# Kernel optimization log

Measured on AMD Instinct MI355X. Metric: run time of the kernel, lower is better.

Reference implementation:

```python
import jax, jax.numpy as jnp
import numpy as np

C_CURV = 0.001
L = 10
N = 16
OMEGA = 1.0
EPS = 1e-6


def _fnmap(x, a0, a, b):
    # x: [M, C]; radial Fourier gate
    r = jnp.maximum(jnp.linalg.norm(x, axis=1, keepdims=True), EPS)  # [M,1]
    n = jnp.arange(1, N + 1, dtype=x.dtype)[None, :]                 # [1,N]
    angle = OMEGA * (r * n)                                          # [M,N]
    f_r = a0 + jnp.cos(angle) @ a[:, None] + jnp.sin(angle) @ b[:, None]  # [M,1]
    return f_r * x


def _log_map_origin(x, c):
    sc = jnp.sqrt(c)
    rn = jnp.maximum(jnp.linalg.norm(x, axis=1, keepdims=True), EPS)
    arg = jnp.minimum(sc * rn, 1.0 - 1e-5)
    return (jnp.arctanh(arg) / (sc * rn)) * x


def _exp_map_origin(v, c):
    sc = jnp.sqrt(c)
    rn = jnp.maximum(jnp.linalg.norm(v, axis=1, keepdims=True), EPS)
    return (jnp.tanh(sc * rn) / (sc * rn)) * v


def setup_inputs() -> dict:
    key = jax.random.key(0)
    ks = jax.random.split(key, 8)
    B, C, H, W = 32, 256, 64, 64
    x = jax.random.normal(ks[0], (B, C, H, W), dtype=jnp.float32) * 0.1
    inp = {
        "x": x,
        "a0_1": jnp.ones((1,), jnp.float32),
        "a_1": jax.random.normal(ks[1], (N,), jnp.float32) * 0.02,
        "b_1": jax.random.normal(ks[2], (N,), jnp.float32) * 0.02,
        "a0_2": jnp.ones((1,), jnp.float32),
        "a_2": jax.random.normal(ks[3], (N,), jnp.float32) * 0.02,
        "b_2": jax.random.normal(ks[4], (N,), jnp.float32) * 0.02,
        "phi": jax.random.normal(ks[5], (C,), jnp.float32) * 0.02,
        "alpha": jnp.ones((1,), jnp.float32),
        "beta": jnp.zeros((1,), jnp.float32),
    }
    return inp


def reference(x, a0_1, a_1, b_1, a0_2, a_2, b_2, phi, alpha, beta):
    B, C, H, W = x.shape
    h0 = jnp.transpose(x, (0, 2, 3, 1)).reshape(-1, C)  # [B*H*W, C]
    u = _log_map_origin(h0, C_CURV)
    u1 = _fnmap(u, a0_1, a_1, b_1)
    U = jnp.fft.rfft(u1, axis=1)                         # [M, C//2+1]
    ang = L * phi
    Hf = jax.lax.complex(jnp.cos(ang), jnp.sin(ang))     # [C]
    V = U * Hf[None, : U.shape[-1]]
    v0 = jnp.fft.irfft(V, n=C, axis=1)
    v1 = _fnmap(v0, a0_2, a_2, b_2)
    y = _exp_map_origin(v1, C_CURV)
    out = alpha * y + beta * h0
    return jnp.transpose(out.reshape(B, H, W, C), (0, 3, 1, 2))
```

## Files before the change

kernel.cpp:

```cpp
#include <hip/hip_runtime.h>
#include <math.h>

typedef __attribute__((ext_vector_type(8))) unsigned short ushort8;
typedef __attribute__((ext_vector_type(8))) __bf16 bf16x8;
typedef __attribute__((ext_vector_type(4))) float f32x4;

constexpr int   CDIM  = 256;
constexpr int   HWSP  = 4096;
constexpr int   PPB   = 64;
constexpr float SQRTC = 0.031622776601683794f;
constexpr float EPSR  = 1e-6f;

__device__ inline unsigned short f2bf(float x) {
    unsigned int u = __float_as_uint(x);
    u += 0x7FFFu + ((u >> 16) & 1u);
    return (unsigned short)(u >> 16);
}

__global__ void build_wpk(const float* __restrict__ phi,
                          unsigned short* __restrict__ wpk) {
    __shared__ float w[256];
    const int d = threadIdx.x;
    {
        const float step = 6.283185307179586f / 256.0f;
        double s = 0.0;
        for (int k = 1; k <= 127; ++k) {
            int kd = (k * d) & 255;
            s += 2.0 * (double)cosf(10.0f * phi[k] + step * (float)kd);
        }
        s += (double)cosf(10.0f * phi[0]);
        double c128 = (double)cosf(10.0f * phi[128]);
        s += (d & 1) ? -c128 : c128;
        w[d] = (float)(s * (1.0 / 256.0));
    }
    __syncthreads();
    const int l = d & 63, q = d >> 6;
    for (int blk = q; blk < 128; blk += 4) {
        const int outc = (blk & 15) * 16 + (l & 15);
        const int ch0  = (blk >> 4) * 32 + (l >> 4) * 8;
        ushort8 u;
        #pragma unroll
        for (int j = 0; j < 8; ++j)
            u[j] = f2bf(w[(outc - (ch0 + j)) & 255]);
        *reinterpret_cast<ushort8*>(&wpk[(size_t)(blk * 64 + l) * 8]) = u;
    }
}

__device__ inline float fourier_gate(float r, float A0,
                                     const float* __restrict__ a,
                                     const float* __restrict__ b) {
    float sn, cs;
    sincosf(r, &sn, &cs);
    float c = cs, s = sn, f = A0;
    #pragma unroll
    for (int n = 0; n < 16; ++n) {
        f = fmaf(a[n], c, f);
        f = fmaf(b[n], s, f);
        float c2 = fmaf(c, cs, -s * sn);
        float s2 = fmaf(s, cs,  c * sn);
        c = c2; s = s2;
    }
    return f;
}

__global__ __launch_bounds__(256, 4)
void fused_mfma(const float* __restrict__ x,
                const float* __restrict__ a0_1, const float* __restrict__ a1,
                const float* __restrict__ b1,
                const float* __restrict__ a0_2, const float* __restrict__ a2,
                const float* __restrict__ b2,
                const float* __restrict__ phi,
                const float* __restrict__ alpha, const float* __restrict__ beta,
                const unsigned short* __restrict__ wpk,
                float* __restrict__ out) {
    __shared__ __align__(16) unsigned short Xl[PPB][CDIM];
    __shared__ __align__(16) float stats[3][4][PPB];
    __shared__ __align__(16) float sobuf[PPB];

    const int t  = threadIdx.x;
    const int l  = t & 63;
    const int g  = t >> 6;
    const int lr = l & 15;
    const int lk = l >> 4;
    const int b  = blockIdx.x >> 6;
    const int s0 = (blockIdx.x & 63) * PPB;
    const float* xb = x + (size_t)b * CDIM * HWSP + s0;

    f32x4 vns = {0.f,0.f,0.f,0.f}, vs0 = {0.f,0.f,0.f,0.f}, vsa = {0.f,0.f,0.f,0.f};
    const int posq = t & 15;
    #pragma unroll
    for (int i = 0; i < 2; ++i) {
        const int co = i * 16 + (t >> 4);
        f32x4 v[8];
        #pragma unroll
        for (int j = 0; j < 8; ++j)
            v[j] = *reinterpret_cast<const f32x4*>(
                       &xb[(size_t)(co * 8 + j) * HWSP + posq * 4]);
        #pragma unroll
        for (int j = 0; j < 8; ++j) {
            vns += v[j] * v[j];
            vs0 += v[j];
            vsa  = (j & 1) ? vsa - v[j] : vsa + v[j];
        }
        #pragma unroll
        for (int r = 0; r < 4; ++r) {
            ushort8 u;
            #pragma unroll
            for (int j = 0; j < 8; ++j) u[j] = f2bf(v[j][r]);
            const int pos = posq * 4 + r;
            *reinterpret_cast<ushort8*>(&Xl[pos][(co * 8) ^ ((pos & 15) << 3)]) = u;
        }
    }
    #pragma unroll
    for (int r = 0; r < 4; ++r) {
        float aa = vns[r], ss = vs0[r], mm = vsa[r];
        aa += __shfl_xor(aa, 16, 64); aa += __shfl_xor(aa, 32, 64);
        ss += __shfl_xor(ss, 16, 64); ss += __shfl_xor(ss, 32, 64);
        mm += __shfl_xor(mm, 16, 64); mm += __shfl_xor(mm, 32, 64);
        vns[r] = aa; vs0[r] = ss; vsa[r] = mm;
    }
    if (lk == 0) {
        *reinterpret_cast<f32x4*>(&stats[0][g][posq * 4]) = vns;
        *reinterpret_cast<f32x4*>(&stats[1][g][posq * 4]) = vs0;
        *reinterpret_cast<f32x4*>(&stats[2][g][posq * 4]) = vsa;
    }
    __syncthreads();

    if (t < PPB) {
        float nsq = stats[0][0][t] + stats[0][1][t] + stats[0][2][t] + stats[0][3][t];
        float S0  = stats[1][0][t] + stats[1][1][t] + stats[1][2][t] + stats[1][3][t];
        float Sa  = stats[2][0][t] + stats[2][1][t] + stats[2][2][t] + stats[2][3][t];
        float sin0 = sinf(10.0f * phi[0]);
        float sinN = sinf(10.0f * phi[128]);
        float n0  = sqrtf(nsq);
        float rn0 = fmaxf(n0, EPSR);
        float arg = fminf(SQRTC * rn0, 1.0f - 1e-5f);
        float ls  = atanhf(arg) / (SQRTC * rn0);
        float r1  = fmaxf(ls * n0, EPSR);
        float s1  = ls * fourier_gate(r1, a0_1[0], a1, b1);
        float dn2 = fmaxf(nsq - (S0 * S0 * sin0 * sin0 + Sa * Sa * sinN * sinN)
                                 * (1.0f / 256.0f), 0.f);
        float nv  = sqrtf(dn2) * fabsf(s1);
        float r2  = fmaxf(nv, EPSR);
        float f2  = fourier_gate(r2, a0_2[0], a2, b2);
        float rn1 = fmaxf(fabsf(f2) * nv, EPSR);
        float es  = tanhf(SQRTC * rn1) / (SQRTC * rn1);
        sobuf[t]  = alpha[0] * es * f2 * s1;
    }

    f32x4 acc[4][4];
    #pragma unroll
    for (int m = 0; m < 4; ++m)
        #pragma unroll
        for (int n = 0; n < 4; ++n)
            acc[m][n] = f32x4{0.f, 0.f, 0.f, 0.f};

    #pragma unroll
    for (int ks = 0; ks < 8; ++ks) {
        const int kb = ks * 32 + lk * 8;
        bf16x8 af[4], bw[4];
        #pragma unroll
        for (int m = 0; m < 4; ++m) {
            const int pos = m * 16 + lr;
            af[m] = __builtin_bit_cast(bf16x8,
                *reinterpret_cast<const ushort8*>(&Xl[pos][kb ^ ((pos & 15) << 3)]));
        }
        #pragma unroll
        for (int n = 0; n < 4; ++n)
            bw[n] = __builtin_bit_cast(bf16x8,
                *reinterpret_cast<const ushort8*>(
                    &wpk[(size_t)((ks * 16 + g * 4 + n) * 64 + l) * 8]));
        #pragma unroll
        for (int m = 0; m < 4; ++m)
            #pragma unroll
            for (int n = 0; n < 4; ++n)
                acc[m][n] = __builtin_amdgcn_mfma_f32_16x16x32_bf16(
                    af[m], bw[n], acc[m][n], 0, 0, 0);
    }
    __syncthreads();

    const float bb = beta[0];
    float* ob = out + (size_t)b * CDIM * HWSP + s0;
    if (bb == 0.f) {
        #pragma unroll
        for (int m = 0; m < 4; ++m) {
            const int p0 = m * 16 + lk * 4;
            const f32x4 sob = *reinterpret_cast<const f32x4*>(&sobuf[p0]);
            #pragma unroll
            for (int n = 0; n < 4; ++n) {
                const int outc = (g * 4 + n) * 16 + lr;
                f32x4 vv = acc[m][n] * sob;
                *reinterpret_cast<f32x4*>(&ob[(size_t)outc * HWSP + p0]) = vv;
            }
        }
    } else {
        #pragma unroll
        for (int m = 0; m < 4; ++m) {
            const int p0 = m * 16 + lk * 4;
            const f32x4 sob = *reinterpret_cast<const f32x4*>(&sobuf[p0]);
            #pragma unroll
            for (int n = 0; n < 4; ++n) {
                const int outc = (g * 4 + n) * 16 + lr;
                const f32x4 xv = *reinterpret_cast<const f32x4*>(
                                     &xb[(size_t)outc * HWSP + p0]);
                f32x4 vv = acc[m][n] * sob + bb * xv;
                *reinterpret_cast<f32x4*>(&ob[(size_t)outc * HWSP + p0]) = vv;
            }
        }
    }
}

extern "C" void kernel_launch(void* const* d_in, const int* in_sizes, int n_in,
                              void* d_out, int out_size, void* d_ws, size_t ws_size,
                              hipStream_t stream) {
    const float* x     = (const float*)d_in[0];
    const float* a0_1  = (const float*)d_in[1];
    const float* a1    = (const float*)d_in[2];
    const float* b1    = (const float*)d_in[3];
    const float* a0_2  = (const float*)d_in[4];
    const float* a2    = (const float*)d_in[5];
    const float* b2    = (const float*)d_in[6];
    const float* phi   = (const float*)d_in[7];
    const float* alpha = (const float*)d_in[8];
    const float* beta  = (const float*)d_in[9];

    unsigned short* wpk = (unsigned short*)d_ws;

    build_wpk<<<1, 256, 0, stream>>>(phi, wpk);

    const int B = in_sizes[0] / (CDIM * HWSP);
    fused_mfma<<<dim3(B * (HWSP / PPB)), dim3(256), 0, stream>>>(
        x, a0_1, a1, b1, a0_2, a2, b2, phi, alpha, beta, wpk, (float*)d_out);
}
```

Baseline: 81.86 us.

## Make blocks persistent over four tiles with prefetch, 512 threads, double-buffered LDS

```diff
diff --git a/kernel.cpp b/kernel.cpp
--- a/kernel.cpp
+++ b/kernel.cpp
@@ -8,6 +8,7 @@
 constexpr int   CDIM  = 256;
 constexpr int   HWSP  = 4096;
 constexpr int   PPB   = 64;
+constexpr int   TPT   = 4;
 constexpr float SQRTC = 0.031622776601683794f;
 constexpr float EPSR  = 1e-6f;
 
@@ -16,6 +17,7 @@
     u += 0x7FFFu + ((u >> 16) & 1u);
     return (unsigned short)(u >> 16);
 }
+__device__ inline int swz(int pos) { return ((pos ^ (pos >> 2)) & 15) << 3; }
 
 __global__ void build_wpk(const float* __restrict__ phi,
                           unsigned short* __restrict__ wpk) {
@@ -63,7 +65,7 @@
     return f;
 }
 
-__global__ __launch_bounds__(256, 4)
+__global__ __launch_bounds__(512, 4)
 void fused_mfma(const float* __restrict__ x,
                 const float* __restrict__ a0_1, const float* __restrict__ a1,
                 const float* __restrict__ b1,
@@ -73,138 +75,154 @@
                 const float* __restrict__ alpha, const float* __restrict__ beta,
                 const unsigned short* __restrict__ wpk,
                 float* __restrict__ out) {
-    __shared__ __align__(16) unsigned short Xl[PPB][CDIM];
-    __shared__ __align__(16) float stats[3][4][PPB];
+    __shared__ __align__(16) unsigned short Xl[2][PPB][CDIM];
+    __shared__ __align__(16) float stats[3][8][PPB];
     __shared__ __align__(16) float sobuf[PPB];
 
-    const int t  = threadIdx.x;
-    const int l  = t & 63;
-    const int g  = t >> 6;
-    const int lr = l & 15;
-    const int lk = l >> 4;
-    const int b  = blockIdx.x >> 6;
-    const int s0 = (blockIdx.x & 63) * PPB;
-    const float* xb = x + (size_t)b * CDIM * HWSP + s0;
-
-    f32x4 vns = {0.f,0.f,0.f,0.f}, vs0 = {0.f,0.f,0.f,0.f}, vsa = {0.f,0.f,0.f,0.f};
+    const int t    = threadIdx.x;
+    const int l    = t & 63;
+    const int w    = t >> 6;
+    const int lr   = l & 15;
+    const int lk   = l >> 4;
     const int posq = t & 15;
-    #pragma unroll
-    for (int i = 0; i < 2; ++i) {
-        const int co = i * 16 + (t >> 4);
-        f32x4 v[8];
+    const int co   = t >> 4;
+
+    const float bb = beta[0];
+    f32x4 v[8];
+
+    auto issue_loads = [&](int tau) {
+        const float* xb = x + (size_t)(tau >> 6) * CDIM * HWSP + (tau & 63) * PPB;
         #pragma unroll
         for (int j = 0; j < 8; ++j)
             v[j] = *reinterpret_cast<const f32x4*>(
                        &xb[(size_t)(co * 8 + j) * HWSP + posq * 4]);
-        #pragma unroll
-        for (int j = 0; j < 8; ++j) {
-            vns += v[j] * v[j];
-            vs0 += v[j];
-            vsa  = (j & 1) ? vsa - v[j] : vsa + v[j];
-        }
-        #pragma unroll
-        for (int r = 0; r < 4; ++r) {
-            ushort8 u;
-            #pragma unroll
-            for (int j = 0; j < 8; ++j) u[j] = f2bf(v[j][r]);
-            const int pos = posq * 4 + r;
-            *reinterpret_cast<ushort8*>(&Xl[pos][(co * 8) ^ ((pos & 15) << 3)]) = u;
-        }
-    }
-    #pragma unroll
-    for (int r = 0; r < 4; ++r) {
-        float aa = vns[r], ss = vs0[r], mm = vsa[r];
-        aa += __shfl_xor(aa, 16, 64); aa += __shfl_xor(aa, 32, 64);
-        ss += __shfl_xor(ss, 16, 64); ss += __shfl_xor(ss, 32, 64);
-        mm += __shfl_xor(mm, 16, 64); mm += __shfl_xor(mm, 32, 64);
-        vns[r] = aa; vs0[r] = ss; vsa[r] = mm;
-    }
-    if (lk == 0) {
-        *reinterpret_cast<f32x4*>(&stats[0][g][posq * 4]) = vns;
-        *reinterpret_cast<f32x4*>(&stats[1][g][posq * 4]) = vs0;
-        *reinterpret_cast<f32x4*>(&stats[2][g][posq * 4]) = vsa;
-    }
-    __syncthreads();
-
-    if (t < PPB) {
-        float nsq = stats[0][0][t] + stats[0][1][t] + stats[0][2][t] + stats[0][3][t];
-        float S0  = stats[1][0][t] + stats[1][1][t] + stats[1][2][t] + stats[1][3][t];
-        float Sa  = stats[2][0][t] + stats[2][1][t] + stats[2][2][t] + stats[2][3][t];
-        float sin0 = sinf(10.0f * phi[0]);
-        float sinN = sinf(10.0f * phi[128]);
-        float n0  = sqrtf(nsq);
-        float rn0 = fmaxf(n0, EPSR);
-        float arg = fminf(SQRTC * rn0, 1.0f - 1e-5f);
-        float ls  = atanhf(arg) / (SQRTC * rn0);
-        float r1  = fmaxf(ls * n0, EPSR);
-        float s1  = ls * fourier_gate(r1, a0_1[0], a1, b1);
-        float dn2 = fmaxf(nsq - (S0 * S0 * sin0 * sin0 + Sa * Sa * sinN * sinN)
-                                 * (1.0f / 256.0f), 0.f);
-        float nv  = sqrtf(dn2) * fabsf(s1);
-        float r2  = fmaxf(nv, EPSR);
-        float f2  = fourier_gate(r2, a0_2[0], a2, b2);
-        float rn1 = fmaxf(fabsf(f2) * nv, EPSR);
-        float es  = tanhf(SQRTC * rn1) / (SQRTC * rn1);
-        sobuf[t]  = alpha[0] * es * f2 * s1;
-    }
-
-    f32x4 acc[4][4];
-    #pragma unroll
-    for (int m = 0; m < 4; ++m)
-        #pragma unroll
-        for (int n = 0; n < 4; ++n)
-            acc[m][n] = f32x4{0.f, 0.f, 0.f, 0.f};
-
-    #pragma unroll
-    for (int ks = 0; ks < 8; ++ks) {
-        const int kb = ks * 32 + lk * 8;
-        bf16x8 af[4], bw[4];
-        #pragma unroll
-        for (int m = 0; m < 4; ++m) {
-            const int pos = m * 16 + lr;
-            af[m] = __builtin_bit_cast(bf16x8,
-                *reinterpret_cast<const ushort8*>(&Xl[pos][kb ^ ((pos & 15) << 3)]));
-        }
-        #pragma unroll
-        for (int n = 0; n < 4; ++n)
-            bw[n] = __builtin_bit_cast(bf16x8,
-                *reinterpret_cast<const ushort8*>(
-                    &wpk[(size_t)((ks * 16 + g * 4 + n) * 64 + l) * 8]));
+    };
+
+    const int tau0 = blockIdx.x * TPT;
+    issue_loads(tau0);
+
+    for (int i = 0; i < TPT; ++i) {
+        const int cur = i & 1;
+        const int tau = tau0 + i;
+        const float* xb = x + (size_t)(tau >> 6) * CDIM * HWSP + (tau & 63) * PPB;
+        float*       ob = out + (size_t)(tau >> 6) * CDIM * HWSP + (tau & 63) * PPB;
+
+        {
+            f32x4 vns = {0,0,0,0}, vs0 = {0,0,0,0}, vsa = {0,0,0,0};
+            #pragma unroll
+            for (int j = 0; j < 8; ++j) {
+                vns += v[j] * v[j];
+                vs0 += v[j];
+                vsa  = (j & 1) ? vsa - v[j] : vsa + v[j];
+            }
+            #pragma unroll
+            for (int r = 0; r < 4; ++r) {
+                ushort8 u;
+                #pragma unroll
+                for (int j = 0; j < 8; ++j) u[j] = f2bf(v[j][r]);
+                const int pos = posq * 4 + r;
+                *reinterpret_cast<ushort8*>(&Xl[cur][pos][(co * 8) ^ swz(pos)]) = u;
+            }
+            #pragma unroll
+            for (int r = 0; r < 4; ++r) {
+                float aa = vns[r], ss = vs0[r], mm = vsa[r];
+                aa += __shfl_xor(aa, 16, 64); aa += __shfl_xor(aa, 32, 64);
+                ss += __shfl_xor(ss, 16, 64); ss += __shfl_xor(ss, 32, 64);
+                mm += __shfl_xor(mm, 16, 64); mm += __shfl_xor(mm, 32, 64);
+                vns[r] = aa; vs0[r] = ss; vsa[r] = mm;
+            }
+            if (lk == 0) {
+                *reinterpret_cast<f32x4*>(&stats[0][w][posq * 4]) = vns;
+                *reinterpret_cast<f32x4*>(&stats[1][w][posq * 4]) = vs0;
+                *reinterpret_cast<f32x4*>(&stats[2][w][posq * 4]) = vsa;
+            }
+        }
+        __syncthreads();
+
+        if (i + 1 < TPT) issue_loads(tau + 1);
+
+        if (t < PPB) {
+            float nsq = 0.f, S0 = 0.f, Sa = 0.f;
+            #pragma unroll
+            for (int q = 0; q < 8; ++q) {
+                nsq += stats[0][q][t];
+                S0  += stats[1][q][t];
+                Sa  += stats[2][q][t];
+            }
+            float sin0 = sinf(10.0f * phi[0]);
+            float sinN = sinf(10.0f * phi[128]);
+            float n0  = sqrtf(nsq);
+            float rn0 = fmaxf(n0, EPSR);
+            float arg = fminf(SQRTC * rn0, 1.0f - 1e-5f);
+            float ls  = atanhf(arg) / (SQRTC * rn0);
+            float r1  = fmaxf(ls * n0, EPSR);
+            float s1  = ls * fourier_gate(r1, a0_1[0], a1, b1);
+            float dn2 = fmaxf(nsq - (S0 * S0 * sin0 * sin0 + Sa * Sa * sinN * sinN)
+                                     * (1.0f / 256.0f), 0.f);
+            float nv  = sqrtf(dn2) * fabsf(s1);
+            float r2  = fmaxf(nv, EPSR);
+            float f2  = fourier_gate(r2, a0_2[0], a2, b2);
+            float rn1 = fmaxf(fabsf(f2) * nv, EPSR);
+            float es  = tanhf(SQRTC * rn1) / (SQRTC * rn1);
+            sobuf[t]  = alpha[0] * es * f2 * s1;
+        }
+
+        f32x4 acc[4][2];
         #pragma unroll
         for (int m = 0; m < 4; ++m)
             #pragma unroll
-            for (int n = 0; n < 4; ++n)
-                acc[m][n] = __builtin_amdgcn_mfma_f32_16x16x32_bf16(
-                    af[m], bw[n], acc[m][n], 0, 0, 0);
-    }
-    __syncthreads();
-
-    const float bb = beta[0];
-    float* ob = out + (size_t)b * CDIM * HWSP + s0;
-    if (bb == 0.f) {
-        #pragma unroll
-        for (int m = 0; m < 4; ++m) {
-            const int p0 = m * 16 + lk * 4;
-            const f32x4 sob = *reinterpret_cast<const f32x4*>(&sobuf[p0]);
-            #pragma unroll
-            for (int n = 0; n < 4; ++n) {
-                const int outc = (g * 4 + n) * 16 + lr;
-                f32x4 vv = acc[m][n] * sob;
-                *reinterpret_cast<f32x4*>(&ob[(size_t)outc * HWSP + p0]) = vv;
-            }
-        }
-    } else {
-        #pragma unroll
-        for (int m = 0; m < 4; ++m) {
-            const int p0 = m * 16 + lk * 4;
-            const f32x4 sob = *reinterpret_cast<const f32x4*>(&sobuf[p0]);
-            #pragma unroll
-            for (int n = 0; n < 4; ++n) {
-                const int outc = (g * 4 + n) * 16 + lr;
-                const f32x4 xv = *reinterpret_cast<const f32x4*>(
-                                     &xb[(size_t)outc * HWSP + p0]);
-                f32x4 vv = acc[m][n] * sob + bb * xv;
-                *reinterpret_cast<f32x4*>(&ob[(size_t)outc * HWSP + p0]) = vv;
+            for (int n = 0; n < 2; ++n)
+                acc[m][n] = f32x4{0.f, 0.f, 0.f, 0.f};
+
+        #pragma unroll
+        for (int ks = 0; ks < 8; ++ks) {
+            const int kb = ks * 32 + lk * 8;
+            bf16x8 af[4], bw[2];
+            #pragma unroll
+            for (int m = 0; m < 4; ++m) {
+                const int pos = m * 16 + lr;
+                af[m] = __builtin_bit_cast(bf16x8,
+                    *reinterpret_cast<const ushort8*>(&Xl[cur][pos][kb ^ swz(pos)]));
+            }
+            #pragma unroll
+            for (int n = 0; n < 2; ++n)
+                bw[n] = __builtin_bit_cast(bf16x8,
+                    *reinterpret_cast<const ushort8*>(
+                        &wpk[(size_t)((ks * 16 + w * 2 + n) * 64 + l) * 8]));
+            #pragma unroll
+            for (int m = 0; m < 4; ++m)
+                #pragma unroll
+                for (int n = 0; n < 2; ++n)
+                    acc[m][n] = __builtin_amdgcn_mfma_f32_16x16x32_bf16(
+                        af[m], bw[n], acc[m][n], 0, 0, 0);
+        }
+        __syncthreads();
+
+        if (bb == 0.f) {
+            #pragma unroll
+            for (int m = 0; m < 4; ++m) {
+                const int p0 = m * 16 + lk * 4;
+                const f32x4 sob = *reinterpret_cast<const f32x4*>(&sobuf[p0]);
+                #pragma unroll
+                for (int n = 0; n < 2; ++n) {
+                    const int outc = (w * 2 + n) * 16 + lr;
+                    f32x4 vv = acc[m][n] * sob;
+                    *reinterpret_cast<f32x4*>(&ob[(size_t)outc * HWSP + p0]) = vv;
+                }
+            }
+        } else {
+            #pragma unroll
+            for (int m = 0; m < 4; ++m) {
+                const int p0 = m * 16 + lk * 4;
+                const f32x4 sob = *reinterpret_cast<const f32x4*>(&sobuf[p0]);
+                #pragma unroll
+                for (int n = 0; n < 2; ++n) {
+                    const int outc = (w * 2 + n) * 16 + lr;
+                    const f32x4 xv = *reinterpret_cast<const f32x4*>(
+                                         &xb[(size_t)outc * HWSP + p0]);
+                    f32x4 vv = acc[m][n] * sob + bb * xv;
+                    *reinterpret_cast<f32x4*>(&ob[(size_t)outc * HWSP + p0]) = vv;
+                }
             }
         }
     }
@@ -229,6 +247,7 @@
     build_wpk<<<1, 256, 0, stream>>>(phi, wpk);
 
     const int B = in_sizes[0] / (CDIM * HWSP);
-    fused_mfma<<<dim3(B * (HWSP / PPB)), dim3(256), 0, stream>>>(
+    const int ntiles = B * (HWSP / PPB);
+    fused_mfma<<<dim3(ntiles / TPT), dim3(512), 0, stream>>>(
         x, a0_1, a1, b1, a0_2, a2, b2, phi, alpha, beta, wpk, (float*)d_out);
 }
```

Result: slower. 172.8 us (+111.1%).

## Stage input via direct global-to-LDS loads in fp32 and halve pixels per block

Applied to the files above, without the earlier changes.

```diff
diff --git a/kernel.cpp b/kernel.cpp
--- a/kernel.cpp
+++ b/kernel.cpp
@@ -7,7 +7,7 @@
 
 constexpr int   CDIM  = 256;
 constexpr int   HWSP  = 4096;
-constexpr int   PPB   = 64;
+constexpr int   PPB   = 32;
 constexpr float SQRTC = 0.031622776601683794f;
 constexpr float EPSR  = 1e-6f;
 
@@ -15,6 +15,12 @@
     unsigned int u = __float_as_uint(x);
     u += 0x7FFFu + ((u >> 16) & 1u);
     return (unsigned short)(u >> 16);
+}
+
+__device__ inline void glds16(const float* g, void* l) {
+    __builtin_amdgcn_global_load_lds(
+        (const __attribute__((address_space(1))) void*)g,
+        (__attribute__((address_space(3))) void*)l, 16, 0, 0);
 }
 
 __global__ void build_wpk(const float* __restrict__ phi,
@@ -73,7 +79,7 @@
                 const float* __restrict__ alpha, const float* __restrict__ beta,
                 const unsigned short* __restrict__ wpk,
                 float* __restrict__ out) {
-    __shared__ __align__(16) unsigned short Xl[PPB][CDIM];
+    __shared__ __align__(16) float Xf32[CDIM][PPB];
     __shared__ __align__(16) float stats[3][4][PPB];
     __shared__ __align__(16) float sobuf[PPB];
 
@@ -82,47 +88,42 @@
     const int g  = t >> 6;
     const int lr = l & 15;
     const int lk = l >> 4;
-    const int b  = blockIdx.x >> 6;
-    const int s0 = (blockIdx.x & 63) * PPB;
+    const int b  = blockIdx.x >> 7;
+    const int s0 = (blockIdx.x & 127) * PPB;
     const float* xb = x + (size_t)b * CDIM * HWSP + s0;
 
-    f32x4 vns = {0.f,0.f,0.f,0.f}, vs0 = {0.f,0.f,0.f,0.f}, vsa = {0.f,0.f,0.f,0.f};
-    const int posq = t & 15;
-    #pragma unroll
-    for (int i = 0; i < 2; ++i) {
-        const int co = i * 16 + (t >> 4);
-        f32x4 v[8];
-        #pragma unroll
-        for (int j = 0; j < 8; ++j)
-            v[j] = *reinterpret_cast<const f32x4*>(
-                       &xb[(size_t)(co * 8 + j) * HWSP + posq * 4]);
+    #pragma unroll
+    for (int i = 0; i < 8; ++i) {
+        const int ch0 = g * 64 + i * 8;
+        const float* gp = xb + (size_t)(ch0 + (l >> 3)) * HWSP + (l & 7) * 4;
+        glds16(gp, &Xf32[ch0][0]);
+    }
+    __syncthreads();
+
+    {
+        const int co   = t >> 3;
+        const int posq = t & 7;
+        f32x4 vns = {0,0,0,0}, vs0 = {0,0,0,0}, vsa = {0,0,0,0};
         #pragma unroll
         for (int j = 0; j < 8; ++j) {
-            vns += v[j] * v[j];
-            vs0 += v[j];
-            vsa  = (j & 1) ? vsa - v[j] : vsa + v[j];
+            f32x4 v = *reinterpret_cast<const f32x4*>(&Xf32[co * 8 + j][posq * 4]);
+            vns += v * v;
+            vs0 += v;
+            vsa  = (j & 1) ? vsa - v : vsa + v;
         }
         #pragma unroll
         for (int r = 0; r < 4; ++r) {
-            ushort8 u;
-            #pragma unroll
-            for (int j = 0; j < 8; ++j) u[j] = f2bf(v[j][r]);
-            const int pos = posq * 4 + r;
-            *reinterpret_cast<ushort8*>(&Xl[pos][(co * 8) ^ ((pos & 15) << 3)]) = u;
-        }
-    }
-    #pragma unroll
-    for (int r = 0; r < 4; ++r) {
-        float aa = vns[r], ss = vs0[r], mm = vsa[r];
-        aa += __shfl_xor(aa, 16, 64); aa += __shfl_xor(aa, 32, 64);
-        ss += __shfl_xor(ss, 16, 64); ss += __shfl_xor(ss, 32, 64);
-        mm += __shfl_xor(mm, 16, 64); mm += __shfl_xor(mm, 32, 64);
-        vns[r] = aa; vs0[r] = ss; vsa[r] = mm;
-    }
-    if (lk == 0) {
-        *reinterpret_cast<f32x4*>(&stats[0][g][posq * 4]) = vns;
-        *reinterpret_cast<f32x4*>(&stats[1][g][posq * 4]) = vs0;
-        *reinterpret_cast<f32x4*>(&stats[2][g][posq * 4]) = vsa;
+            float aa = vns[r], ss = vs0[r], mm = vsa[r];
+            aa += __shfl_xor(aa, 8, 64); aa += __shfl_xor(aa, 16, 64); aa += __shfl_xor(aa, 32, 64);
+            ss += __shfl_xor(ss, 8, 64); ss += __shfl_xor(ss, 16, 64); ss += __shfl_xor(ss, 32, 64);
+            mm += __shfl_xor(mm, 8, 64); mm += __shfl_xor(mm, 16, 64); mm += __shfl_xor(mm, 32, 64);
+            vns[r] = aa; vs0[r] = ss; vsa[r] = mm;
+        }
+        if (l < 8) {
+            *reinterpret_cast<f32x4*>(&stats[0][g][l * 4]) = vns;
+            *reinterpret_cast<f32x4*>(&stats[1][g][l * 4]) = vs0;
+            *reinterpret_cast<f32x4*>(&stats[2][g][l * 4]) = vsa;
+        }
     }
     __syncthreads();
 
@@ -148,22 +149,25 @@
         sobuf[t]  = alpha[0] * es * f2 * s1;
     }
 
-    f32x4 acc[4][4];
-    #pragma unroll
-    for (int m = 0; m < 4; ++m)
+    f32x4 acc[2][4];
+    #pragma unroll
+    for (int m = 0; m < 2; ++m)
         #pragma unroll
         for (int n = 0; n < 4; ++n)
             acc[m][n] = f32x4{0.f, 0.f, 0.f, 0.f};
 
     #pragma unroll
     for (int ks = 0; ks < 8; ++ks) {
-        const int kb = ks * 32 + lk * 8;
-        bf16x8 af[4], bw[4];
-        #pragma unroll
-        for (int m = 0; m < 4; ++m) {
+        const int ch0 = ks * 32 + lk * 8;
+        bf16x8 af[2], bw[4];
+        #pragma unroll
+        for (int m = 0; m < 2; ++m) {
             const int pos = m * 16 + lr;
-            af[m] = __builtin_bit_cast(bf16x8,
-                *reinterpret_cast<const ushort8*>(&Xl[pos][kb ^ ((pos & 15) << 3)]));
+            bf16x8 u;
+            #pragma unroll
+            for (int j = 0; j < 8; ++j)
+                u[j] = (__bf16)Xf32[ch0 + j][pos];
+            af[m] = u;
         }
         #pragma unroll
         for (int n = 0; n < 4; ++n)
@@ -171,7 +175,7 @@
                 *reinterpret_cast<const ushort8*>(
                     &wpk[(size_t)((ks * 16 + g * 4 + n) * 64 + l) * 8]));
         #pragma unroll
-        for (int m = 0; m < 4; ++m)
+        for (int m = 0; m < 2; ++m)
             #pragma unroll
             for (int n = 0; n < 4; ++n)
                 acc[m][n] = __builtin_amdgcn_mfma_f32_16x16x32_bf16(
@@ -183,7 +187,7 @@
     float* ob = out + (size_t)b * CDIM * HWSP + s0;
     if (bb == 0.f) {
         #pragma unroll
-        for (int m = 0; m < 4; ++m) {
+        for (int m = 0; m < 2; ++m) {
             const int p0 = m * 16 + lk * 4;
             const f32x4 sob = *reinterpret_cast<const f32x4*>(&sobuf[p0]);
             #pragma unroll
@@ -195,7 +199,7 @@
         }
     } else {
         #pragma unroll
-        for (int m = 0; m < 4; ++m) {
+        for (int m = 0; m < 2; ++m) {
             const int p0 = m * 16 + lk * 4;
             const f32x4 sob = *reinterpret_cast<const f32x4*>(&sobuf[p0]);
             #pragma unroll
```

Measured after the change: 84.12 us. 1.03x slower.
